# Performance work log

Measured on AMD Instinct MI355X. Metric: run time of the kernel, lower is better.

The kernel has to match this reference:

```python
import jax, jax.numpy as jnp
import numpy as np

N_NODES = 50000
N_EDGES = 800000
D_FEAT = 96
OUT_DIM = 96


def setup_inputs() -> dict:
    key = jax.random.key(0)
    k1, k2, k3, k4 = jax.random.split(key, 4)
    x = jax.random.normal(k1, (N_NODES, D_FEAT), dtype=jnp.float32)
    W = jax.random.normal(k2, (D_FEAT, OUT_DIM), dtype=jnp.float32) / np.sqrt(D_FEAT)
    b = jnp.zeros((OUT_DIM,), dtype=jnp.float32)
    src = jax.random.randint(k3, (N_EDGES,), 0, N_NODES, dtype=jnp.int64)
    dst = jax.random.randint(k4, (N_EDGES,), 0, N_NODES, dtype=jnp.int64)
    return {"x": x, "W": W, "b": b, "src": src, "dst": dst}


def reference(x, W, b, src, dst):
    # GCNConv: symmetric degree normalization, transform-then-aggregate.
    ones = jnp.ones(src.shape[0], dtype=x.dtype)
    deg_out = jax.ops.segment_sum(ones, src, num_segments=N_NODES)  # [N]
    deg_in = jax.ops.segment_sum(ones, dst, num_segments=N_NODES)   # [N]
    inv_sqrt_out = jnp.where(deg_out > 0, jax.lax.rsqrt(deg_out), 0.0)
    inv_sqrt_in = jnp.where(deg_in > 0, jax.lax.rsqrt(deg_in), 0.0)

    h = x @ W  # [N, out_dim] - transform first (cheap GEMM)
    coef = inv_sqrt_out[src] * inv_sqrt_in[dst]         # [E]
    msg = h[src] * coef[:, None]                         # [E, out_dim] gather
    agg = jax.ops.segment_sum(msg, dst, num_segments=N_NODES)  # scatter-reduce
    return agg + b
```

## Files before the change

kernel.cpp:

```cpp
#include <hip/hip_runtime.h>

#define N_NODES 50000
#define N_EDGES 800000
#define DFEAT 96

#define RBITS  14
#define RSIZE  16384
#define NRANGE 4
#define NCHUNK 64
#define CHUNK_E (N_EDGES / NCHUNK)
#define HF_BLOCKS (NRANGE * NCHUNK)
#define NB 196

typedef short bf16x8 __attribute__((ext_vector_type(8)));
typedef float f32x4  __attribute__((ext_vector_type(4)));

__device__ __forceinline__ unsigned bpack(float a, float b) {
    unsigned ua = __float_as_uint(a);
    unsigned ub = __float_as_uint(b);
    ua = (ua + 0x7FFFu + ((ua >> 16) & 1u)) >> 16;
    ub = (ub + 0x7FFFu + ((ub >> 16) & 1u)) >> 16;
    return ua | (ub << 16);
}
__device__ __forceinline__ unsigned short b1(float a) {
    unsigned u = __float_as_uint(a);
    u = (u + 0x7FFFu + ((u >> 16) & 1u)) >> 16;
    return (unsigned short)u;
}

__global__ __launch_bounds__(512) void deg_hist_kernel(
    const int* __restrict__ src, const int* __restrict__ dst,
    unsigned* __restrict__ ptab) {
    __shared__ unsigned hh[RSIZE];
    int tid = threadIdx.x;
    int r = blockIdx.x & (NRANGE - 1);
    int c = blockIdx.x >> 2;
    for (int i = tid; i < RSIZE; i += 512) hh[i] = 0;
    __syncthreads();
    int lo = r << RBITS;
    const int4* s4 = (const int4*)(src + c * CHUNK_E);
    const int4* d4 = (const int4*)(dst + c * CHUNK_E);
    for (int i = tid; i < CHUNK_E / 4; i += 512) {
        int4 s = s4[i];
        int4 d = d4[i];
        unsigned a;
        a = (unsigned)(s.x - lo); if (a < RSIZE) atomicAdd(&hh[a], 1u);
        a = (unsigned)(s.y - lo); if (a < RSIZE) atomicAdd(&hh[a], 1u);
        a = (unsigned)(s.z - lo); if (a < RSIZE) atomicAdd(&hh[a], 1u);
        a = (unsigned)(s.w - lo); if (a < RSIZE) atomicAdd(&hh[a], 1u);
        a = (unsigned)(d.x - lo); if (a < RSIZE) atomicAdd(&hh[a], 0x10000u);
        a = (unsigned)(d.y - lo); if (a < RSIZE) atomicAdd(&hh[a], 0x10000u);
        a = (unsigned)(d.z - lo); if (a < RSIZE) atomicAdd(&hh[a], 0x10000u);
        a = (unsigned)(d.w - lo); if (a < RSIZE) atomicAdd(&hh[a], 0x10000u);
    }
    __syncthreads();
    unsigned* pt = ptab + ((size_t)blockIdx.x << RBITS);
    for (int i = tid; i < RSIZE; i += 512) pt[i] = hh[i];
}

__global__ __launch_bounds__(256) void deg_reduce_kernel(
    const unsigned* __restrict__ ptab, unsigned short* __restrict__ pfx,
    int* __restrict__ deg_out, int* __restrict__ deg_in,
    int* __restrict__ bsum) {
    __shared__ int ws[4];
    int tid = threadIdx.x;
    int n = blockIdx.x * 256 + tid;
    int so = 0, si = 0;
    if (n < N_NODES) {
        int r = n >> RBITS, bin = n & (RSIZE - 1);
        #pragma unroll 8
        for (int c = 0; c < NCHUNK; ++c) {
            size_t idx = (((size_t)(c * NRANGE + r)) << RBITS) + bin;
            unsigned v = ptab[idx];
            so += (int)(v & 0xffffu);
            pfx[idx] = (unsigned short)si;
            si += (int)(v >> 16);
        }
        deg_out[n] = so;
        deg_in[n]  = si;
    }
    int v = si;
    #pragma unroll
    for (int off = 32; off; off >>= 1) v += __shfl_down(v, off, 64);
    if ((tid & 63) == 0) ws[tid >> 6] = v;
    __syncthreads();
    if (tid == 0) bsum[blockIdx.x] = ws[0] + ws[1] + ws[2] + ws[3];
}

__global__ __launch_bounds__(256) void scan_final_kernel(
    const int* __restrict__ deg, const int* __restrict__ bsum,
    int* __restrict__ offs, int nb) {
    __shared__ int wsum[4];
    __shared__ int sbase;
    int tid = threadIdx.x, lane = tid & 63, wave = tid >> 6;
    int i = blockIdx.x * 256 + tid;
    int v = (i < N_NODES) ? deg[i] : 0;
    int x = v;
    #pragma unroll
    for (int off = 1; off < 64; off <<= 1) {
        int t = __shfl_up(x, off, 64);
        if (lane >= off) x += t;
    }
    if (lane == 63) wsum[wave] = x;
    if (wave == 0) {
        int s = 0;
        for (int j = lane; j < blockIdx.x; j += 64) s += bsum[j];
        #pragma unroll
        for (int off = 32; off; off >>= 1) s += __shfl_down(s, off, 64);
        if (lane == 0) sbase = s;
    }
    if (blockIdx.x == gridDim.x - 1 && wave == 1) {
        int s = 0;
        for (int j = lane; j < nb; j += 64) s += bsum[j];
        #pragma unroll
        for (int off = 32; off; off >>= 1) s += __shfl_down(s, off, 64);
        if (lane == 0) offs[N_NODES] = s;
    }
    __syncthreads();
    int wb = sbase;
    for (int w = 0; w < wave; ++w) wb += wsum[w];
    if (i < N_NODES) offs[i] = wb + x - v;
}

#define GROWS 128
#define NGB ((N_NODES + GROWS - 1) / GROWS)
#define TLD 104

union FGSm {
    int cur[RSIZE];
    struct {
        unsigned short WT[96 * TLD];
        unsigned short xA[GROWS * TLD];
    } g;
};

__global__ __launch_bounds__(512) void fill_gemm_kernel(
    const int* __restrict__ src, const int* __restrict__ dst,
    const int* __restrict__ offs, const unsigned short* __restrict__ pfx,
    int* __restrict__ csr_src,
    const float* __restrict__ x, const float* __restrict__ W,
    const int* __restrict__ deg_out, unsigned short* __restrict__ h, int nrows) {
    __shared__ FGSm sm;
    int tid = threadIdx.x;

    if (blockIdx.x < HF_BLOCKS) {
        int r = blockIdx.x & (NRANGE - 1);
        int c = blockIdx.x >> 2;
        int lo = r << RBITS;
        const unsigned short* pf = pfx + ((size_t)blockIdx.x << RBITS);
        for (int i = tid; i < RSIZE; i += 512) {
            int gi = lo + i;
            int o = (gi < N_NODES) ? offs[gi] : 0;
            sm.cur[i] = o + (int)pf[i];
        }
        __syncthreads();
        const int4* s4 = (const int4*)(src + c * CHUNK_E);
        const int4* d4 = (const int4*)(dst + c * CHUNK_E);
        for (int i = tid; i < CHUNK_E / 4; i += 512) {
            int4 s = s4[i];
            int4 d = d4[i];
            unsigned a;
            a = (unsigned)(d.x - lo); if (a < RSIZE) csr_src[atomicAdd(&sm.cur[a], 1)] = s.x;
            a = (unsigned)(d.y - lo); if (a < RSIZE) csr_src[atomicAdd(&sm.cur[a], 1)] = s.y;
            a = (unsigned)(d.z - lo); if (a < RSIZE) csr_src[atomicAdd(&sm.cur[a], 1)] = s.z;
            a = (unsigned)(d.w - lo); if (a < RSIZE) csr_src[atomicAdd(&sm.cur[a], 1)] = s.w;
        }
        return;
    }

    int r0 = (blockIdx.x - HF_BLOCKS) * GROWS;

    for (int i = tid; i < 48 * 96; i += 512) {
        int k2 = i / 96, n = i - k2 * 96;
        float w0 = W[(size_t)(2 * k2) * 96 + n];
        float w1 = W[(size_t)(2 * k2 + 1) * 96 + n];
        *(unsigned*)&sm.g.WT[n * TLD + 2 * k2] = bpack(w0, w1);
    }
    for (int i = tid; i < GROWS * 24; i += 512) {
        int m = i / 24, k4 = i - m * 24;
        int row = r0 + m; if (row >= nrows) row = nrows - 1;
        float4 v = *(const float4*)&x[(size_t)row * 96 + 4 * k4];
        *(unsigned*)&sm.g.xA[m * TLD + 4 * k4]     = bpack(v.x, v.y);
        *(unsigned*)&sm.g.xA[m * TLD + 4 * k4 + 2] = bpack(v.z, v.w);
    }
    __syncthreads();

    int lane = tid & 63, wave = tid >> 6;
    int m16 = lane & 15;
    int g = lane >> 4;
    int rbase = wave * 16;

    bf16x8 afrag[3];
    #pragma unroll
    for (int ks = 0; ks < 3; ++ks)
        afrag[ks] = *(const bf16x8*)&sm.g.xA[(rbase + m16) * TLD + ks * 32 + g * 8];

    f32x4 acc[6];
    #pragma unroll
    for (int nt = 0; nt < 6; ++nt) {
        f32x4 c = {0.f, 0.f, 0.f, 0.f};
        #pragma unroll
        for (int ks = 0; ks < 3; ++ks) {
            bf16x8 bfrag = *(const bf16x8*)&sm.g.WT[(nt * 16 + m16) * TLD + ks * 32 + g * 8];
            c = __builtin_amdgcn_mfma_f32_16x16x32_bf16(afrag[ks], bfrag, c, 0, 0, 0);
        }
        acc[nt] = c;
    }

    float s[4];
    #pragma unroll
    for (int r = 0; r < 4; ++r) {
        int row = r0 + rbase + g * 4 + r;
        int d = (row < nrows) ? deg_out[row] : 1;
        s[r] = (d > 0) ? rsqrtf((float)d) : 0.f;
    }
    #pragma unroll
    for (int nt = 0; nt < 6; ++nt) {
        #pragma unroll
        for (int r = 0; r < 4; ++r) {
            int row = r0 + rbase + g * 4 + r;
            if (row < nrows)
                h[(size_t)row * 96 + nt * 16 + m16] = b1(acc[nt][r] * s[r]);
        }
    }
}

__device__ __forceinline__ void upadd(float* a, uint4 q) {
    a[0] += __uint_as_float(q.x << 16);
    a[1] += __uint_as_float(q.x & 0xffff0000u);
    a[2] += __uint_as_float(q.y << 16);
    a[3] += __uint_as_float(q.y & 0xffff0000u);
    a[4] += __uint_as_float(q.z << 16);
    a[5] += __uint_as_float(q.z & 0xffff0000u);
    a[6] += __uint_as_float(q.w << 16);
    a[7] += __uint_as_float(q.w & 0xffff0000u);
}

#define AGG_NODES 16
#define IDX_CAP 2048
#define NPASS 4
__global__ __launch_bounds__(256) void agg_kernel(
    const unsigned short* __restrict__ h, const int* __restrict__ csr_src,
    const int* __restrict__ offs, const float* __restrict__ b,
    float* __restrict__ out) {
    __shared__ int sh_idx[IDX_CAP];
    __shared__ int sh_off[AGG_NODES + 1];
    int tid = threadIdx.x;
    int n0 = blockIdx.x * AGG_NODES;
    if (tid <= AGG_NODES) sh_off[tid] = offs[n0 + tid];
    __syncthreads();
    int s0 = sh_off[0];
    int len = sh_off[AGG_NODES] - s0;
    bool lds_ok = (len <= IDX_CAP);
    if (lds_ok) {
        for (int i = tid; i < len; i += 256) sh_idx[i] = csr_src[s0 + i];
    }
    __syncthreads();

    int node = tid >> 4;
    int lane16 = tid & 15;
    int j = lane16 & 3;
    int q = lane16 >> 2;
    int start = sh_off[node], end = sh_off[node + 1];
    float acc[24];
    #pragma unroll
    for (int i = 0; i < 24; ++i) acc[i] = 0.f;
    const uint4* hb = (const uint4*)h;

    for (int pass = 0; pass < NPASS; ++pass) {
        int e = start + q;
        for (; e + 4 < end; e += 8) {
            int i0 = lds_ok ? sh_idx[e - s0] : csr_src[e];
            int i1 = lds_ok ? sh_idx[e + 4 - s0] : csr_src[e + 4];
            if ((i0 >> RBITS) == pass) {
                size_t b0 = (size_t)i0 * 12 + j;
                uint4 q0 = hb[b0], q1 = hb[b0 + 4], q2 = hb[b0 + 8];
                upadd(acc + 0, q0); upadd(acc + 8, q1); upadd(acc + 16, q2);
            }
            if ((i1 >> RBITS) == pass) {
                size_t b1 = (size_t)i1 * 12 + j;
                uint4 p0 = hb[b1], p1 = hb[b1 + 4], p2 = hb[b1 + 8];
                upadd(acc + 0, p0); upadd(acc + 8, p1); upadd(acc + 16, p2);
            }
        }
        if (e < end) {
            int i0 = lds_ok ? sh_idx[e - s0] : csr_src[e];
            if ((i0 >> RBITS) == pass) {
                size_t b0 = (size_t)i0 * 12 + j;
                uint4 q0 = hb[b0], q1 = hb[b0 + 4], q2 = hb[b0 + 8];
                upadd(acc + 0, q0); upadd(acc + 8, q1); upadd(acc + 16, q2);
            }
        }
    }
    #pragma unroll
    for (int i = 0; i < 24; ++i) {
        acc[i] += __shfl_xor(acc[i], 4, 64);
        acc[i] += __shfl_xor(acc[i], 8, 64);
    }
    if (q != 0) return;
    float inv = (end > start) ? rsqrtf((float)(end - start)) : 0.f;
    int n = n0 + node;
    #pragma unroll
    for (int g = 0; g < 3; ++g) {
        int slot = j + 4 * g;
        float4 bb0 = *(const float4*)(b + 8 * slot);
        float4 bb1 = *(const float4*)(b + 8 * slot + 4);
        float4 r0, r1;
        r0.x = acc[g * 8 + 0] * inv + bb0.x;
        r0.y = acc[g * 8 + 1] * inv + bb0.y;
        r0.z = acc[g * 8 + 2] * inv + bb0.z;
        r0.w = acc[g * 8 + 3] * inv + bb0.w;
        r1.x = acc[g * 8 + 4] * inv + bb1.x;
        r1.y = acc[g * 8 + 5] * inv + bb1.y;
        r1.z = acc[g * 8 + 6] * inv + bb1.z;
        r1.w = acc[g * 8 + 7] * inv + bb1.w;
        float4* o = (float4*)(out + (size_t)n * DFEAT + 8 * slot);
        o[0] = r0; o[1] = r1;
    }
}

extern "C" void kernel_launch(void* const* d_in, const int* in_sizes, int n_in,
                              void* d_out, int out_size, void* d_ws, size_t ws_size,
                              hipStream_t stream) {
    const float* x  = (const float*)d_in[0];
    const float* W  = (const float*)d_in[1];
    const float* b  = (const float*)d_in[2];
    const int*   src = (const int*)d_in[3];
    const int*   dst = (const int*)d_in[4];
    float* out = (float*)d_out;

    int* deg_out = (int*)d_ws;
    int* deg_in  = deg_out + N_NODES;
    int* offs    = deg_in + N_NODES;
    int* csr_src = offs + N_NODES + 1;
    int* bsum    = csr_src + N_EDGES;
    size_t off1 = (((size_t)(3 * N_NODES + 1 + N_EDGES + 256)) * 4 + 255) & ~(size_t)255;
    unsigned* ptab = (unsigned*)((char*)d_ws + off1);
    size_t off2 = off1 + ((size_t)HF_BLOCKS << RBITS) * 4;
    unsigned short* pfx = (unsigned short*)((char*)d_ws + off2);
    size_t off3 = (off2 + ((size_t)HF_BLOCKS << RBITS) * 2 + 255) & ~(size_t)255;
    unsigned short* h = (unsigned short*)((char*)d_ws + off3);

    deg_hist_kernel<<<HF_BLOCKS, 512, 0, stream>>>(src, dst, ptab);
    deg_reduce_kernel<<<NB, 256, 0, stream>>>(ptab, pfx, deg_out, deg_in, bsum);
    scan_final_kernel<<<NB, 256, 0, stream>>>(deg_in, bsum, offs, NB);
    fill_gemm_kernel<<<HF_BLOCKS + NGB, 512, 0, stream>>>(
        src, dst, offs, pfx, csr_src, x, W, deg_out, h, N_NODES);
    agg_kernel<<<N_NODES / AGG_NODES, 256, 0, stream>>>(h, csr_src, offs, b, out);
}
```

Before: 149.1 us.

## Build CSR with global atomics instead of LDS range histograms and chunk prefixes

Replaces the range-partitioned LDS histogram, chunk reduction and per-chunk prefix tables with a zero kernel, direct global atomic degree counting, and a single scan that recomputes block bases from the degree array. The CSR fill uses global atomic cursors in place of LDS cursors, and the aggregation drops its four range passes so all neighbours are gathered in one pass. The aim is to remove the large partial tables' traffic, a launch, and the multi-pass aggregation loop. In exchange it adds contended global atomics and a nondeterministic edge order within each row, and each scan block rereads the whole degree prefix.

```diff
diff --git a/kernel.cpp b/kernel.cpp
--- a/kernel.cpp
+++ b/kernel.cpp
@@ -4,13 +4,11 @@
 #define N_EDGES 800000
 #define DFEAT 96
 
-#define RBITS  14
-#define RSIZE  16384
-#define NRANGE 4
-#define NCHUNK 64
-#define CHUNK_E (N_EDGES / NCHUNK)
-#define HF_BLOCKS (NRANGE * NCHUNK)
 #define NB 196
+#define FB 64
+#define GROWS 128
+#define NGB ((N_NODES + GROWS - 1) / GROWS)
+#define TLD 104
 
 typedef short bf16x8 __attribute__((ext_vector_type(8)));
 typedef float f32x4  __attribute__((ext_vector_type(4)));
@@ -28,160 +26,101 @@
     return (unsigned short)u;
 }
 
-__global__ __launch_bounds__(512) void deg_hist_kernel(
+__global__ __launch_bounds__(256) void zero_kernel(int4* __restrict__ p, int n4) {
+    int i = blockIdx.x * 256 + threadIdx.x;
+    if (i < n4) p[i] = make_int4(0, 0, 0, 0);
+}
+
+__global__ __launch_bounds__(256) void deg_kernel(
     const int* __restrict__ src, const int* __restrict__ dst,
-    unsigned* __restrict__ ptab) {
-    __shared__ unsigned hh[RSIZE];
-    int tid = threadIdx.x;
-    int r = blockIdx.x & (NRANGE - 1);
-    int c = blockIdx.x >> 2;
-    for (int i = tid; i < RSIZE; i += 512) hh[i] = 0;
-    __syncthreads();
-    int lo = r << RBITS;
-    const int4* s4 = (const int4*)(src + c * CHUNK_E);
-    const int4* d4 = (const int4*)(dst + c * CHUNK_E);
-    for (int i = tid; i < CHUNK_E / 4; i += 512) {
-        int4 s = s4[i];
-        int4 d = d4[i];
-        unsigned a;
-        a = (unsigned)(s.x - lo); if (a < RSIZE) atomicAdd(&hh[a], 1u);
-        a = (unsigned)(s.y - lo); if (a < RSIZE) atomicAdd(&hh[a], 1u);
-        a = (unsigned)(s.z - lo); if (a < RSIZE) atomicAdd(&hh[a], 1u);
-        a = (unsigned)(s.w - lo); if (a < RSIZE) atomicAdd(&hh[a], 1u);
-        a = (unsigned)(d.x - lo); if (a < RSIZE) atomicAdd(&hh[a], 0x10000u);
-        a = (unsigned)(d.y - lo); if (a < RSIZE) atomicAdd(&hh[a], 0x10000u);
-        a = (unsigned)(d.z - lo); if (a < RSIZE) atomicAdd(&hh[a], 0x10000u);
-        a = (unsigned)(d.w - lo); if (a < RSIZE) atomicAdd(&hh[a], 0x10000u);
-    }
-    __syncthreads();
-    unsigned* pt = ptab + ((size_t)blockIdx.x << RBITS);
-    for (int i = tid; i < RSIZE; i += 512) pt[i] = hh[i];
-}
-
-__global__ __launch_bounds__(256) void deg_reduce_kernel(
-    const unsigned* __restrict__ ptab, unsigned short* __restrict__ pfx,
-    int* __restrict__ deg_out, int* __restrict__ deg_in,
-    int* __restrict__ bsum) {
-    __shared__ int ws[4];
-    int tid = threadIdx.x;
-    int n = blockIdx.x * 256 + tid;
-    int so = 0, si = 0;
-    if (n < N_NODES) {
-        int r = n >> RBITS, bin = n & (RSIZE - 1);
-        #pragma unroll 8
-        for (int c = 0; c < NCHUNK; ++c) {
-            size_t idx = (((size_t)(c * NRANGE + r)) << RBITS) + bin;
-            unsigned v = ptab[idx];
-            so += (int)(v & 0xffffu);
-            pfx[idx] = (unsigned short)si;
-            si += (int)(v >> 16);
-        }
-        deg_out[n] = so;
-        deg_in[n]  = si;
-    }
-    int v = si;
-    #pragma unroll
-    for (int off = 32; off; off >>= 1) v += __shfl_down(v, off, 64);
-    if ((tid & 63) == 0) ws[tid >> 6] = v;
-    __syncthreads();
-    if (tid == 0) bsum[blockIdx.x] = ws[0] + ws[1] + ws[2] + ws[3];
-}
-
-__global__ __launch_bounds__(256) void scan_final_kernel(
-    const int* __restrict__ deg, const int* __restrict__ bsum,
-    int* __restrict__ offs, int nb) {
-    __shared__ int wsum[4];
+    int* __restrict__ deg_out, int* __restrict__ deg_in) {
+    int i = blockIdx.x * 256 + threadIdx.x;
+    if (i >= N_EDGES / 4) return;
+    const int4* s4 = (const int4*)src;
+    const int4* d4 = (const int4*)dst;
+    int4 s = s4[i];
+    int4 d = d4[i];
+    atomicAdd(&deg_out[s.x], 1); atomicAdd(&deg_out[s.y], 1);
+    atomicAdd(&deg_out[s.z], 1); atomicAdd(&deg_out[s.w], 1);
+    atomicAdd(&deg_in[d.x], 1);  atomicAdd(&deg_in[d.y], 1);
+    atomicAdd(&deg_in[d.z], 1);  atomicAdd(&deg_in[d.w], 1);
+}
+
+__global__ __launch_bounds__(256) void scan_kernel(
+    const int* __restrict__ deg, int* __restrict__ offs, int* __restrict__ cur) {
+    __shared__ int red[4];
+    __shared__ int wsc[4];
     __shared__ int sbase;
     int tid = threadIdx.x, lane = tid & 63, wave = tid >> 6;
     int i = blockIdx.x * 256 + tid;
     int v = (i < N_NODES) ? deg[i] : 0;
+
+    int lim = blockIdx.x * 256;
+    int s = 0;
+    for (int j = tid; j < lim; j += 256) s += deg[j];
+    #pragma unroll
+    for (int off = 32; off; off >>= 1) s += __shfl_down(s, off, 64);
+    if (lane == 0) red[wave] = s;
+    __syncthreads();
+    if (tid == 0) sbase = red[0] + red[1] + red[2] + red[3];
+
     int x = v;
     #pragma unroll
     for (int off = 1; off < 64; off <<= 1) {
         int t = __shfl_up(x, off, 64);
         if (lane >= off) x += t;
     }
-    if (lane == 63) wsum[wave] = x;
-    if (wave == 0) {
-        int s = 0;
-        for (int j = lane; j < blockIdx.x; j += 64) s += bsum[j];
-        #pragma unroll
-        for (int off = 32; off; off >>= 1) s += __shfl_down(s, off, 64);
-        if (lane == 0) sbase = s;
-    }
-    if (blockIdx.x == gridDim.x - 1 && wave == 1) {
-        int s = 0;
-        for (int j = lane; j < nb; j += 64) s += bsum[j];
-        #pragma unroll
-        for (int off = 32; off; off >>= 1) s += __shfl_down(s, off, 64);
-        if (lane == 0) offs[N_NODES] = s;
-    }
-    __syncthreads();
+    if (lane == 63) wsc[wave] = x;
+    __syncthreads();
+
     int wb = sbase;
-    for (int w = 0; w < wave; ++w) wb += wsum[w];
-    if (i < N_NODES) offs[i] = wb + x - v;
-}
-
-#define GROWS 128
-#define NGB ((N_NODES + GROWS - 1) / GROWS)
-#define TLD 104
-
-union FGSm {
-    int cur[RSIZE];
-    struct {
-        unsigned short WT[96 * TLD];
-        unsigned short xA[GROWS * TLD];
-    } g;
+    for (int w = 0; w < wave; ++w) wb += wsc[w];
+    int o = wb + x - v;
+    if (i < N_NODES) { offs[i] = o; cur[i] = o; }
+    if (blockIdx.x == gridDim.x - 1 && tid == 255) offs[N_NODES] = wb + x;
+}
+
+struct GSm {
+    unsigned short WT[96 * TLD];
+    unsigned short xA[GROWS * TLD];
 };
 
 __global__ __launch_bounds__(512) void fill_gemm_kernel(
     const int* __restrict__ src, const int* __restrict__ dst,
-    const int* __restrict__ offs, const unsigned short* __restrict__ pfx,
-    int* __restrict__ csr_src,
+    int* __restrict__ cur, int* __restrict__ csr_src,
     const float* __restrict__ x, const float* __restrict__ W,
     const int* __restrict__ deg_out, unsigned short* __restrict__ h, int nrows) {
-    __shared__ FGSm sm;
+    __shared__ GSm sm;
     int tid = threadIdx.x;
 
-    if (blockIdx.x < HF_BLOCKS) {
-        int r = blockIdx.x & (NRANGE - 1);
-        int c = blockIdx.x >> 2;
-        int lo = r << RBITS;
-        const unsigned short* pf = pfx + ((size_t)blockIdx.x << RBITS);
-        for (int i = tid; i < RSIZE; i += 512) {
-            int gi = lo + i;
-            int o = (gi < N_NODES) ? offs[gi] : 0;
-            sm.cur[i] = o + (int)pf[i];
-        }
-        __syncthreads();
-        const int4* s4 = (const int4*)(src + c * CHUNK_E);
-        const int4* d4 = (const int4*)(dst + c * CHUNK_E);
-        for (int i = tid; i < CHUNK_E / 4; i += 512) {
+    if (blockIdx.x < FB) {
+        const int4* s4 = (const int4*)src;
+        const int4* d4 = (const int4*)dst;
+        for (int i = blockIdx.x * 512 + tid; i < N_EDGES / 4; i += FB * 512) {
             int4 s = s4[i];
             int4 d = d4[i];
-            unsigned a;
-            a = (unsigned)(d.x - lo); if (a < RSIZE) csr_src[atomicAdd(&sm.cur[a], 1)] = s.x;
-            a = (unsigned)(d.y - lo); if (a < RSIZE) csr_src[atomicAdd(&sm.cur[a], 1)] = s.y;
-            a = (unsigned)(d.z - lo); if (a < RSIZE) csr_src[atomicAdd(&sm.cur[a], 1)] = s.z;
-            a = (unsigned)(d.w - lo); if (a < RSIZE) csr_src[atomicAdd(&sm.cur[a], 1)] = s.w;
+            csr_src[atomicAdd(&cur[d.x], 1)] = s.x;
+            csr_src[atomicAdd(&cur[d.y], 1)] = s.y;
+            csr_src[atomicAdd(&cur[d.z], 1)] = s.z;
+            csr_src[atomicAdd(&cur[d.w], 1)] = s.w;
         }
         return;
     }
 
-    int r0 = (blockIdx.x - HF_BLOCKS) * GROWS;
+    int r0 = (blockIdx.x - FB) * GROWS;
 
     for (int i = tid; i < 48 * 96; i += 512) {
         int k2 = i / 96, n = i - k2 * 96;
         float w0 = W[(size_t)(2 * k2) * 96 + n];
         float w1 = W[(size_t)(2 * k2 + 1) * 96 + n];
-        *(unsigned*)&sm.g.WT[n * TLD + 2 * k2] = bpack(w0, w1);
+        *(unsigned*)&sm.WT[n * TLD + 2 * k2] = bpack(w0, w1);
     }
     for (int i = tid; i < GROWS * 24; i += 512) {
         int m = i / 24, k4 = i - m * 24;
         int row = r0 + m; if (row >= nrows) row = nrows - 1;
         float4 v = *(const float4*)&x[(size_t)row * 96 + 4 * k4];
-        *(unsigned*)&sm.g.xA[m * TLD + 4 * k4]     = bpack(v.x, v.y);
-        *(unsigned*)&sm.g.xA[m * TLD + 4 * k4 + 2] = bpack(v.z, v.w);
+        *(unsigned*)&sm.xA[m * TLD + 4 * k4]     = bpack(v.x, v.y);
+        *(unsigned*)&sm.xA[m * TLD + 4 * k4 + 2] = bpack(v.z, v.w);
     }
     __syncthreads();
 
@@ -193,7 +132,7 @@
     bf16x8 afrag[3];
     #pragma unroll
     for (int ks = 0; ks < 3; ++ks)
-        afrag[ks] = *(const bf16x8*)&sm.g.xA[(rbase + m16) * TLD + ks * 32 + g * 8];
+        afrag[ks] = *(const bf16x8*)&sm.xA[(rbase + m16) * TLD + ks * 32 + g * 8];
 
     f32x4 acc[6];
     #pragma unroll
@@ -201,18 +140,18 @@
         f32x4 c = {0.f, 0.f, 0.f, 0.f};
         #pragma unroll
         for (int ks = 0; ks < 3; ++ks) {
-            bf16x8 bfrag = *(const bf16x8*)&sm.g.WT[(nt * 16 + m16) * TLD + ks * 32 + g * 8];
+            bf16x8 bfrag = *(const bf16x8*)&sm.WT[(nt * 16 + m16) * TLD + ks * 32 + g * 8];
             c = __builtin_amdgcn_mfma_f32_16x16x32_bf16(afrag[ks], bfrag, c, 0, 0, 0);
         }
         acc[nt] = c;
     }
 
-    float s[4];
+    float sc[4];
     #pragma unroll
     for (int r = 0; r < 4; ++r) {
         int row = r0 + rbase + g * 4 + r;
         int d = (row < nrows) ? deg_out[row] : 1;
-        s[r] = (d > 0) ? rsqrtf((float)d) : 0.f;
+        sc[r] = (d > 0) ? rsqrtf((float)d) : 0.f;
     }
     #pragma unroll
     for (int nt = 0; nt < 6; ++nt) {
@@ -220,7 +159,7 @@
         for (int r = 0; r < 4; ++r) {
             int row = r0 + rbase + g * 4 + r;
             if (row < nrows)
-                h[(size_t)row * 96 + nt * 16 + m16] = b1(acc[nt][r] * s[r]);
+                h[(size_t)row * 96 + nt * 16 + m16] = b1(acc[nt][r] * sc[r]);
         }
     }
 }
@@ -238,7 +177,6 @@
 
 #define AGG_NODES 16
 #define IDX_CAP 2048
-#define NPASS 4
 __global__ __launch_bounds__(256) void agg_kernel(
     const unsigned short* __restrict__ h, const int* __restrict__ csr_src,
     const int* __restrict__ offs, const float* __restrict__ b,
@@ -267,30 +205,22 @@
     for (int i = 0; i < 24; ++i) acc[i] = 0.f;
     const uint4* hb = (const uint4*)h;
 
-    for (int pass = 0; pass < NPASS; ++pass) {
-        int e = start + q;
-        for (; e + 4 < end; e += 8) {
-            int i0 = lds_ok ? sh_idx[e - s0] : csr_src[e];
-            int i1 = lds_ok ? sh_idx[e + 4 - s0] : csr_src[e + 4];
-            if ((i0 >> RBITS) == pass) {
-                size_t b0 = (size_t)i0 * 12 + j;
-                uint4 q0 = hb[b0], q1 = hb[b0 + 4], q2 = hb[b0 + 8];
-                upadd(acc + 0, q0); upadd(acc + 8, q1); upadd(acc + 16, q2);
-            }
-            if ((i1 >> RBITS) == pass) {
-                size_t b1 = (size_t)i1 * 12 + j;
-                uint4 p0 = hb[b1], p1 = hb[b1 + 4], p2 = hb[b1 + 8];
-                upadd(acc + 0, p0); upadd(acc + 8, p1); upadd(acc + 16, p2);
-            }
-        }
-        if (e < end) {
-            int i0 = lds_ok ? sh_idx[e - s0] : csr_src[e];
-            if ((i0 >> RBITS) == pass) {
-                size_t b0 = (size_t)i0 * 12 + j;
-                uint4 q0 = hb[b0], q1 = hb[b0 + 4], q2 = hb[b0 + 8];
-                upadd(acc + 0, q0); upadd(acc + 8, q1); upadd(acc + 16, q2);
-            }
-        }
+    int e = start + q;
+    for (; e + 4 < end; e += 8) {
+        int i0 = lds_ok ? sh_idx[e - s0] : csr_src[e];
+        int i1 = lds_ok ? sh_idx[e + 4 - s0] : csr_src[e + 4];
+        size_t b0 = (size_t)i0 * 12 + j;
+        size_t b1 = (size_t)i1 * 12 + j;
+        uint4 q0 = hb[b0], q1 = hb[b0 + 4], q2 = hb[b0 + 8];
+        uint4 p0 = hb[b1], p1 = hb[b1 + 4], p2 = hb[b1 + 8];
+        upadd(acc + 0, q0); upadd(acc + 8, q1); upadd(acc + 16, q2);
+        upadd(acc + 0, p0); upadd(acc + 8, p1); upadd(acc + 16, p2);
+    }
+    if (e < end) {
+        int i0 = lds_ok ? sh_idx[e - s0] : csr_src[e];
+        size_t b0 = (size_t)i0 * 12 + j;
+        uint4 q0 = hb[b0], q1 = hb[b0 + 4], q2 = hb[b0 + 8];
+        upadd(acc + 0, q0); upadd(acc + 8, q1); upadd(acc + 16, q2);
     }
     #pragma unroll
     for (int i = 0; i < 24; ++i) {
@@ -332,19 +262,15 @@
     int* deg_out = (int*)d_ws;
     int* deg_in  = deg_out + N_NODES;
     int* offs    = deg_in + N_NODES;
-    int* csr_src = offs + N_NODES + 1;
-    int* bsum    = csr_src + N_EDGES;
-    size_t off1 = (((size_t)(3 * N_NODES + 1 + N_EDGES + 256)) * 4 + 255) & ~(size_t)255;
-    unsigned* ptab = (unsigned*)((char*)d_ws + off1);
-    size_t off2 = off1 + ((size_t)HF_BLOCKS << RBITS) * 4;
-    unsigned short* pfx = (unsigned short*)((char*)d_ws + off2);
-    size_t off3 = (off2 + ((size_t)HF_BLOCKS << RBITS) * 2 + 255) & ~(size_t)255;
+    int* cur     = offs + N_NODES + 4;
+    int* csr_src = cur + N_NODES;
+    size_t off3 = (((size_t)(4 * N_NODES + 8 + N_EDGES)) * 4 + 255) & ~(size_t)255;
     unsigned short* h = (unsigned short*)((char*)d_ws + off3);
 
-    deg_hist_kernel<<<HF_BLOCKS, 512, 0, stream>>>(src, dst, ptab);
-    deg_reduce_kernel<<<NB, 256, 0, stream>>>(ptab, pfx, deg_out, deg_in, bsum);
-    scan_final_kernel<<<NB, 256, 0, stream>>>(deg_in, bsum, offs, NB);
-    fill_gemm_kernel<<<HF_BLOCKS + NGB, 512, 0, stream>>>(
-        src, dst, offs, pfx, csr_src, x, W, deg_out, h, N_NODES);
+    zero_kernel<<<(2 * N_NODES / 4 + 255) / 256, 256, 0, stream>>>((int4*)deg_out, 2 * N_NODES / 4);
+    deg_kernel<<<(N_EDGES / 4 + 255) / 256, 256, 0, stream>>>(src, dst, deg_out, deg_in);
+    scan_kernel<<<NB, 256, 0, stream>>>(deg_in, offs, cur);
+    fill_gemm_kernel<<<FB + NGB, 512, 0, stream>>>(
+        src, dst, cur, csr_src, x, W, deg_out, h, N_NODES);
     agg_kernel<<<N_NODES / AGG_NODES, 256, 0, stream>>>(h, csr_src, offs, b, out);
 }
```

Result: slower. 246.6 us (+65.4%).

## Pack degree histograms into 8-bit counts and drop multi-pass aggregation

Applied to the files above, without the earlier changes.

The degree histogram now packs out/in counts as 8-bit fields, two nodes per 32-bit LDS word. This halves LDS use and the partial-table traffic between histogram and reduce. The CSR fill keeps 16-bit packed rank counters in LDS and reads the node offset from global memory per edge, instead of preloading full 32-bit cursors. The aggregation kernel drops its 4-pass source-range filtering, so each edge index is read once and gathered unconditionally, trading the intended L2 locality for fewer index reads and branches. The 8-bit per-chunk counts would overflow if a node got more than 255 edges in one chunk, which random inputs make unlikely.

```diff
diff --git a/kernel.cpp b/kernel.cpp
--- a/kernel.cpp
+++ b/kernel.cpp
@@ -6,6 +6,7 @@
 
 #define RBITS  14
 #define RSIZE  16384
+#define HWORDS (RSIZE / 2)
 #define NRANGE 4
 #define NCHUNK 64
 #define CHUNK_E (N_EDGES / NCHUNK)
@@ -31,11 +32,11 @@
 __global__ __launch_bounds__(512) void deg_hist_kernel(
     const int* __restrict__ src, const int* __restrict__ dst,
     unsigned* __restrict__ ptab) {
-    __shared__ unsigned hh[RSIZE];
+    __shared__ unsigned hh[HWORDS];
     int tid = threadIdx.x;
     int r = blockIdx.x & (NRANGE - 1);
     int c = blockIdx.x >> 2;
-    for (int i = tid; i < RSIZE; i += 512) hh[i] = 0;
+    for (int i = tid; i < HWORDS; i += 512) hh[i] = 0;
     __syncthreads();
     int lo = r << RBITS;
     const int4* s4 = (const int4*)(src + c * CHUNK_E);
@@ -44,18 +45,18 @@
         int4 s = s4[i];
         int4 d = d4[i];
         unsigned a;
-        a = (unsigned)(s.x - lo); if (a < RSIZE) atomicAdd(&hh[a], 1u);
-        a = (unsigned)(s.y - lo); if (a < RSIZE) atomicAdd(&hh[a], 1u);
-        a = (unsigned)(s.z - lo); if (a < RSIZE) atomicAdd(&hh[a], 1u);
-        a = (unsigned)(s.w - lo); if (a < RSIZE) atomicAdd(&hh[a], 1u);
-        a = (unsigned)(d.x - lo); if (a < RSIZE) atomicAdd(&hh[a], 0x10000u);
-        a = (unsigned)(d.y - lo); if (a < RSIZE) atomicAdd(&hh[a], 0x10000u);
-        a = (unsigned)(d.z - lo); if (a < RSIZE) atomicAdd(&hh[a], 0x10000u);
-        a = (unsigned)(d.w - lo); if (a < RSIZE) atomicAdd(&hh[a], 0x10000u);
-    }
-    __syncthreads();
-    unsigned* pt = ptab + ((size_t)blockIdx.x << RBITS);
-    for (int i = tid; i < RSIZE; i += 512) pt[i] = hh[i];
+        a = (unsigned)(s.x - lo); if (a < RSIZE) atomicAdd(&hh[a >> 1], 1u << ((a & 1) << 4));
+        a = (unsigned)(s.y - lo); if (a < RSIZE) atomicAdd(&hh[a >> 1], 1u << ((a & 1) << 4));
+        a = (unsigned)(s.z - lo); if (a < RSIZE) atomicAdd(&hh[a >> 1], 1u << ((a & 1) << 4));
+        a = (unsigned)(s.w - lo); if (a < RSIZE) atomicAdd(&hh[a >> 1], 1u << ((a & 1) << 4));
+        a = (unsigned)(d.x - lo); if (a < RSIZE) atomicAdd(&hh[a >> 1], 0x100u << ((a & 1) << 4));
+        a = (unsigned)(d.y - lo); if (a < RSIZE) atomicAdd(&hh[a >> 1], 0x100u << ((a & 1) << 4));
+        a = (unsigned)(d.z - lo); if (a < RSIZE) atomicAdd(&hh[a >> 1], 0x100u << ((a & 1) << 4));
+        a = (unsigned)(d.w - lo); if (a < RSIZE) atomicAdd(&hh[a >> 1], 0x100u << ((a & 1) << 4));
+    }
+    __syncthreads();
+    unsigned* pt = ptab + ((size_t)blockIdx.x << (RBITS - 1));
+    for (int i = tid; i < HWORDS; i += 512) pt[i] = hh[i];
 }
 
 __global__ __launch_bounds__(256) void deg_reduce_kernel(
@@ -68,13 +69,13 @@
     int so = 0, si = 0;
     if (n < N_NODES) {
         int r = n >> RBITS, bin = n & (RSIZE - 1);
+        int w = bin >> 1, sh = (bin & 1) << 4;
         #pragma unroll 8
         for (int c = 0; c < NCHUNK; ++c) {
-            size_t idx = (((size_t)(c * NRANGE + r)) << RBITS) + bin;
-            unsigned v = ptab[idx];
-            so += (int)(v & 0xffffu);
-            pfx[idx] = (unsigned short)si;
-            si += (int)(v >> 16);
+            unsigned v = (ptab[(((size_t)(c * NRANGE + r)) << (RBITS - 1)) + w] >> sh) & 0xffffu;
+            so += (int)(v & 0xffu);
+            pfx[(((size_t)(c * NRANGE + r)) << RBITS) + bin] = (unsigned short)si;
+            si += (int)(v >> 8);
         }
         deg_out[n] = so;
         deg_in[n]  = si;
@@ -127,7 +128,7 @@
 #define TLD 104
 
 union FGSm {
-    int cur[RSIZE];
+    unsigned cur[HWORDS];
     struct {
         unsigned short WT[96 * TLD];
         unsigned short xA[GROWS * TLD];
@@ -148,22 +149,39 @@
         int c = blockIdx.x >> 2;
         int lo = r << RBITS;
         const unsigned short* pf = pfx + ((size_t)blockIdx.x << RBITS);
-        for (int i = tid; i < RSIZE; i += 512) {
-            int gi = lo + i;
-            int o = (gi < N_NODES) ? offs[gi] : 0;
-            sm.cur[i] = o + (int)pf[i];
-        }
+        for (int i = tid; i < HWORDS; i += 512)
+            sm.cur[i] = *(const unsigned*)&pf[2 * i];
         __syncthreads();
         const int4* s4 = (const int4*)(src + c * CHUNK_E);
         const int4* d4 = (const int4*)(dst + c * CHUNK_E);
         for (int i = tid; i < CHUNK_E / 4; i += 512) {
             int4 s = s4[i];
             int4 d = d4[i];
-            unsigned a;
-            a = (unsigned)(d.x - lo); if (a < RSIZE) csr_src[atomicAdd(&sm.cur[a], 1)] = s.x;
-            a = (unsigned)(d.y - lo); if (a < RSIZE) csr_src[atomicAdd(&sm.cur[a], 1)] = s.y;
-            a = (unsigned)(d.z - lo); if (a < RSIZE) csr_src[atomicAdd(&sm.cur[a], 1)] = s.z;
-            a = (unsigned)(d.w - lo); if (a < RSIZE) csr_src[atomicAdd(&sm.cur[a], 1)] = s.w;
+            unsigned a, old, rank;
+            a = (unsigned)(d.x - lo);
+            if (a < RSIZE) {
+                old = atomicAdd(&sm.cur[a >> 1], 1u << ((a & 1) << 4));
+                rank = (old >> ((a & 1) << 4)) & 0xffffu;
+                csr_src[offs[lo + a] + rank] = s.x;
+            }
+            a = (unsigned)(d.y - lo);
+            if (a < RSIZE) {
+                old = atomicAdd(&sm.cur[a >> 1], 1u << ((a & 1) << 4));
+                rank = (old >> ((a & 1) << 4)) & 0xffffu;
+                csr_src[offs[lo + a] + rank] = s.y;
+            }
+            a = (unsigned)(d.z - lo);
+            if (a < RSIZE) {
+                old = atomicAdd(&sm.cur[a >> 1], 1u << ((a & 1) << 4));
+                rank = (old >> ((a & 1) << 4)) & 0xffffu;
+                csr_src[offs[lo + a] + rank] = s.z;
+            }
+            a = (unsigned)(d.w - lo);
+            if (a < RSIZE) {
+                old = atomicAdd(&sm.cur[a >> 1], 1u << ((a & 1) << 4));
+                rank = (old >> ((a & 1) << 4)) & 0xffffu;
+                csr_src[offs[lo + a] + rank] = s.w;
+            }
         }
         return;
     }
@@ -207,12 +225,12 @@
         acc[nt] = c;
     }
 
-    float s[4];
+    float sc[4];
     #pragma unroll
     for (int r = 0; r < 4; ++r) {
         int row = r0 + rbase + g * 4 + r;
         int d = (row < nrows) ? deg_out[row] : 1;
-        s[r] = (d > 0) ? rsqrtf((float)d) : 0.f;
+        sc[r] = (d > 0) ? rsqrtf((float)d) : 0.f;
     }
     #pragma unroll
     for (int nt = 0; nt < 6; ++nt) {
@@ -220,7 +238,7 @@
         for (int r = 0; r < 4; ++r) {
             int row = r0 + rbase + g * 4 + r;
             if (row < nrows)
-                h[(size_t)row * 96 + nt * 16 + m16] = b1(acc[nt][r] * s[r]);
+                h[(size_t)row * 96 + nt * 16 + m16] = b1(acc[nt][r] * sc[r]);
         }
     }
 }
@@ -238,7 +256,6 @@
 
 #define AGG_NODES 16
 #define IDX_CAP 2048
-#define NPASS 4
 __global__ __launch_bounds__(256) void agg_kernel(
     const unsigned short* __restrict__ h, const int* __restrict__ csr_src,
     const int* __restrict__ offs, const float* __restrict__ b,
@@ -267,30 +284,22 @@
     for (int i = 0; i < 24; ++i) acc[i] = 0.f;
     const uint4* hb = (const uint4*)h;
 
-    for (int pass = 0; pass < NPASS; ++pass) {
-        int e = start + q;
-        for (; e + 4 < end; e += 8) {
-            int i0 = lds_ok ? sh_idx[e - s0] : csr_src[e];
-            int i1 = lds_ok ? sh_idx[e + 4 - s0] : csr_src[e + 4];
-            if ((i0 >> RBITS) == pass) {
-                size_t b0 = (size_t)i0 * 12 + j;
-                uint4 q0 = hb[b0], q1 = hb[b0 + 4], q2 = hb[b0 + 8];
-                upadd(acc + 0, q0); upadd(acc + 8, q1); upadd(acc + 16, q2);
-            }
-            if ((i1 >> RBITS) == pass) {
-                size_t b1 = (size_t)i1 * 12 + j;
-                uint4 p0 = hb[b1], p1 = hb[b1 + 4], p2 = hb[b1 + 8];
-                upadd(acc + 0, p0); upadd(acc + 8, p1); upadd(acc + 16, p2);
-            }
-        }
-        if (e < end) {
-            int i0 = lds_ok ? sh_idx[e - s0] : csr_src[e];
-            if ((i0 >> RBITS) == pass) {
-                size_t b0 = (size_t)i0 * 12 + j;
-                uint4 q0 = hb[b0], q1 = hb[b0 + 4], q2 = hb[b0 + 8];
-                upadd(acc + 0, q0); upadd(acc + 8, q1); upadd(acc + 16, q2);
-            }
-        }
+    int e = start + q;
+    for (; e + 4 < end; e += 8) {
+        int i0 = lds_ok ? sh_idx[e - s0] : csr_src[e];
+        int i1 = lds_ok ? sh_idx[e + 4 - s0] : csr_src[e + 4];
+        size_t b0 = (size_t)i0 * 12 + j;
+        size_t b1 = (size_t)i1 * 12 + j;
+        uint4 q0 = hb[b0], q1 = hb[b0 + 4], q2 = hb[b0 + 8];
+        uint4 p0 = hb[b1], p1 = hb[b1 + 4], p2 = hb[b1 + 8];
+        upadd(acc + 0, q0); upadd(acc + 8, q1); upadd(acc + 16, q2);
+        upadd(acc + 0, p0); upadd(acc + 8, p1); upadd(acc + 16, p2);
+    }
+    if (e < end) {
+        int i0 = lds_ok ? sh_idx[e - s0] : csr_src[e];
+        size_t b0 = (size_t)i0 * 12 + j;
+        uint4 q0 = hb[b0], q1 = hb[b0 + 4], q2 = hb[b0 + 8];
+        upadd(acc + 0, q0); upadd(acc + 8, q1); upadd(acc + 16, q2);
     }
     #pragma unroll
     for (int i = 0; i < 24; ++i) {
@@ -336,7 +345,7 @@
     int* bsum    = csr_src + N_EDGES;
     size_t off1 = (((size_t)(3 * N_NODES + 1 + N_EDGES + 256)) * 4 + 255) & ~(size_t)255;
     unsigned* ptab = (unsigned*)((char*)d_ws + off1);
-    size_t off2 = off1 + ((size_t)HF_BLOCKS << RBITS) * 4;
+    size_t off2 = off1 + ((size_t)HF_BLOCKS << (RBITS - 1)) * 4;
     unsigned short* pfx = (unsigned short*)((char*)d_ws + off2);
     size_t off3 = (off2 + ((size_t)HF_BLOCKS << RBITS) * 2 + 255) & ~(size_t)255;
     unsigned short* h = (unsigned short*)((char*)d_ws + off3);
```

After: 134.5 us. 1.11x faster.
